# Kernel tuning notes

Measured on AMD Instinct MI355X. Metric: run time of the kernel, lower is better.

## Reference

```python
import jax, jax.numpy as jnp
import numpy as np

DIM = 1024
HEADS = 8
DIM_HEAD = 64
INNER = HEADS * DIM_HEAD  # 512
N_PATCHES = 256
SCALE = DIM_HEAD ** -0.5


def setup_inputs() -> dict:
    key = jax.random.key(0)
    ks = jax.random.split(key, 6)
    s = lambda fan_in: 1.0 / np.sqrt(fan_in)
    return {
        "x": jax.random.normal(ks[0], (64, N_PATCHES, DIM), dtype=jnp.float32),
        "Wq": jax.random.normal(ks[1], (DIM, INNER), dtype=jnp.float32) * s(DIM),
        "Wkv": jax.random.normal(ks[2], (DIM, 2 * INNER), dtype=jnp.float32) * s(DIM),
        "Wout": jax.random.normal(ks[3], (INNER, DIM), dtype=jnp.float32) * s(INNER),
        "bout": jax.random.normal(ks[4], (DIM,), dtype=jnp.float32) * 0.01,
        "Wspec": jax.random.normal(ks[5], (N_PATCHES, 3 * N_PATCHES), dtype=jnp.float32) * s(N_PATCHES),
    }


def reference(x, Wq, Wkv, Wout, bout, Wspec):
    b, n, d = x.shape
    # ---- spatial: single center-query attention ----
    x_center = x[:, n // 2, :]                      # [b, d]
    q = (x_center @ Wq).reshape(b, HEADS, DIM_HEAD)  # [b, h, dh]
    kv = x @ Wkv                                     # [b, n, 2*inner]
    k, v = jnp.split(kv, 2, axis=-1)
    k = k.reshape(b, n, HEADS, DIM_HEAD).transpose(0, 2, 1, 3)  # [b, h, n, dh]
    v = v.reshape(b, n, HEADS, DIM_HEAD).transpose(0, 2, 1, 3)
    logits = jnp.einsum('bhd,bhnd->bhn', q, k) * SCALE
    attn = jax.nn.softmax(logits, axis=-1)           # [b, h, n]
    out = jnp.einsum('bhn,bhnd->bhd', attn, v).reshape(b, INNER)
    # torch expands attn over n identical rows BEFORE to_out; the rows are
    # identical, so broadcasting the projected row is the same math.
    spatial = out @ Wout + bout                      # [b, d]
    spatial_out = jnp.broadcast_to(spatial[:, None, :], (b, n, d))
    # ---- spectral: attention over transposed (feature) axis ----
    x_t = x.transpose(0, 2, 1)                       # [b, d, n]
    qkv = x_t @ Wspec                                # [b, d, 3n]
    q_s, k_s, v_s = jnp.split(qkv, 3, axis=-1)       # v_s unused (as in source)
    spec_logits = jnp.einsum('bin,bjn->bij', q_s, k_s) * SCALE  # [b, d, d]
    spec_weights = jax.nn.softmax(spec_logits, axis=-1)
    return jnp.einsum('bnd,bde->bne', spatial_out, spec_weights)
```

## Files before the change

### kernel.cpp

```cpp
#include <hip/hip_runtime.h>
#include <hip/hip_bf16.h>
#include <cstdint>

typedef _Float16 f16;
typedef _Float16 half8 __attribute__((ext_vector_type(8)));
typedef float f32x4 __attribute__((ext_vector_type(4)));

#define SCALE 0.125f

#define GLL(src, dst) __builtin_amdgcn_global_load_lds( \
    (const __attribute__((address_space(1))) unsigned int*)(src), \
    (__attribute__((address_space(3))) unsigned int*)(dst), 16, 0, 0)

#define GLD(dst, addr) asm volatile("global_load_dwordx4 %0, %1, off" \
    : "=&v"(dst) : "v"(addr) : "memory")

__global__ __launch_bounds__(256) void prep_xT(const float* __restrict__ x, f16* __restrict__ xT) {
  __shared__ f16 tile[32][33];
  int b = blockIdx.z, nt = blockIdx.y, dt = blockIdx.x;
  int c = threadIdx.x & 31, rp = threadIdx.x >> 5;
  const float* xb = x + ((size_t)b*256 + nt*32)*1024 + dt*32;
#pragma unroll
  for (int p = 0; p < 4; ++p) { int r = p*8 + rp; tile[r][c] = (f16)xb[(size_t)r*1024 + c]; }
  __syncthreads();
  f16* o = xT + ((size_t)b*1024 + dt*32)*256 + nt*32;
#pragma unroll
  for (int p = 0; p < 4; ++p) { int r = p*8 + rp; o[(size_t)r*256 + c] = tile[c][r]; }
}

__global__ __launch_bounds__(256) void prep_Wspec16(const float* __restrict__ W, f16* __restrict__ Wt) {
  int row = blockIdx.x, t = threadIdx.x;
  Wt[(size_t)row*512 + t]       = (f16)W[(size_t)row*768 + t];
  Wt[(size_t)row*512 + 256 + t] = (f16)W[(size_t)row*768 + 256 + t];
}

template<int KSTEPS, int AST, int BST, int CST, bool SCALEQ>
__global__ __launch_bounds__(256) void gemm128(const f16* __restrict__ Ag, const f16* __restrict__ Bg,
                                               f16* __restrict__ Cg, size_t aB, size_t bB, size_t cB) {
  __shared__ f16 As[2][128*32];
  __shared__ f16 Bs[2][128*32];
  const f16* A = Ag + (size_t)blockIdx.z*aB;
  const f16* B = Bg + (size_t)blockIdx.z*bB;
  f16* C = Cg + (size_t)blockIdx.z*cB;
  int t = threadIdx.x, lane = t & 63, wave = t >> 6;
  int l15 = lane & 15, l4 = lane >> 4;
  int wm = wave & 1, wn = wave >> 1;
  size_t m0 = (size_t)blockIdx.x*128, n0 = (size_t)blockIdx.y*128;
  f32x4 acc[4][4];
#pragma unroll
  for (int i=0;i<4;++i)
#pragma unroll
    for (int j=0;j<4;++j) acc[i][j] = (f32x4){0.f,0.f,0.f,0.f};
  int rowS[2], chS[2];
#pragma unroll
  for (int c=0;c<2;++c) {
    int slot = c*256 + t;
    rowS[c] = slot >> 2;
    chS[c]  = (slot & 3) ^ ((slot >> 3) & 3);
  }
  int pc = (l4 ^ ((l15 >> 1) & 3)) * 8;

  auto STAGE = [&](int buf, int ks) {
    int k0 = ks*32;
#pragma unroll
    for (int c=0;c<2;++c) {
      GLL(A + (m0 + rowS[c])*(size_t)AST + k0 + chS[c]*8, &As[buf][(c*256 + wave*64)*8]);
      GLL(B + (n0 + rowS[c])*(size_t)BST + k0 + chS[c]*8, &Bs[buf][(c*256 + wave*64)*8]);
    }
  };

  STAGE(0, 0);
#pragma unroll 2
  for (int ks = 0; ks < KSTEPS; ++ks) {
    int cur = ks & 1;
    if (ks + 1 < KSTEPS) {
      STAGE(cur ^ 1, ks + 1);
      asm volatile("s_waitcnt vmcnt(4)" ::: "memory");
    } else {
      asm volatile("s_waitcnt vmcnt(0)" ::: "memory");
    }
    __builtin_amdgcn_s_barrier();
    __builtin_amdgcn_sched_barrier(0);
    half8 a[4], bb[4];
    const f16* Af = &As[cur][(wm*64 + l15)*32 + pc];
    const f16* Bf = &Bs[cur][(wn*64 + l15)*32 + pc];
#pragma unroll
    for (int mi=0;mi<4;++mi) a[mi]  = *(const half8*)(Af + mi*16*32);
#pragma unroll
    for (int ni=0;ni<4;++ni) bb[ni] = *(const half8*)(Bf + ni*16*32);
    __builtin_amdgcn_s_setprio(1);
#pragma unroll
    for (int mi=0;mi<4;++mi)
#pragma unroll
      for (int ni=0;ni<4;++ni)
        acc[mi][ni] = __builtin_amdgcn_mfma_f32_16x16x32_f16(a[mi], bb[ni], acc[mi][ni], 0,0,0);
    __builtin_amdgcn_s_setprio(0);
    __builtin_amdgcn_sched_barrier(0);
    __builtin_amdgcn_s_barrier();
  }
  float cscale = SCALEQ ? SCALE : 1.0f;
#pragma unroll
  for (int mi=0;mi<4;++mi)
#pragma unroll
    for (int ni=0;ni<4;++ni)
#pragma unroll
      for (int j=0;j<4;++j) {
        size_t row = m0 + wm*64 + mi*16 + 4*l4 + j;
        size_t col = n0 + wn*64 + ni*16 + l15;
        C[row*CST + col] = (f16)(acc[mi][ni][j] * cscale);
      }
}

__global__ __launch_bounds__(256) void qk(const float* __restrict__ x, const float* __restrict__ Wq,
                                          float* __restrict__ qbuf) {
  int b = blockIdx.x, h = blockIdx.y;
  int t = threadIdx.x;
  __shared__ float xc[1024];
  __shared__ float part[4][64];
  const float* xcg = x + ((size_t)b*256 + 128)*1024;
#pragma unroll
  for (int i = 0; i < 4; ++i) xc[t + 256*i] = xcg[t + 256*i];
  __syncthreads();
  int d = t & 63, chunk = t >> 6;
  float s = 0.f;
  const float* wq = Wq + (size_t)(chunk*256)*512 + h*64 + d;
#pragma unroll 8
  for (int c = 0; c < 256; ++c) s += xc[chunk*256 + c] * wq[(size_t)c*512];
  part[chunk][d] = s;
  __syncthreads();
  if (t < 64) qbuf[(size_t)b*512 + h*64 + t] = part[0][t]+part[1][t]+part[2][t]+part[3][t];
}

__global__ __launch_bounds__(256) void uk(const float* __restrict__ Wkv, const float* __restrict__ qbuf,
                                          f16* __restrict__ u16) {
  int h = blockIdx.x, dc = blockIdx.y;
  int t = threadIdx.x;
  __shared__ float Wk[32][64];
  __shared__ float qT[64][65];
  {
    int j = t & 63, g = t >> 6;
#pragma unroll
    for (int rr = 0; rr < 8; ++rr) {
      int dd = g*8 + rr;
      Wk[dd][j] = Wkv[(size_t)(dc*32 + dd)*1024 + h*64 + j];
    }
#pragma unroll
    for (int rr = 0; rr < 16; ++rr) {
      int bb = g*16 + rr;
      qT[j][bb] = qbuf[(size_t)bb*512 + h*64 + j];
    }
  }
  __syncthreads();
  int b = t & 63, dq = t >> 6;
#pragma unroll
  for (int i = 0; i < 8; ++i) {
    int dd = dq*8 + i;
    float s = 0.f;
#pragma unroll 8
    for (int j = 0; j < 64; ++j) s += qT[j][b] * Wk[dd][j];
    u16[((size_t)b*16 + h)*1024 + dc*32 + dd] = (f16)s;
  }
}

__global__ __launch_bounds__(64) void lgk(const float* __restrict__ x, const f16* __restrict__ u16,
                                          float* __restrict__ logitbuf) {
  int mt = blockIdx.x, b = blockIdx.y;
  int lane = threadIdx.x, l15 = lane & 15, l4 = lane >> 4;
  const float* Ap = x + ((size_t)b*256 + mt*16 + l15)*1024 + 8*l4;
  const f16* Bp = u16 + ((size_t)b*16 + l15)*1024 + 8*l4;
  f32x4 acc = (f32x4){0.f,0.f,0.f,0.f};
#pragma unroll 8
  for (int ks = 0; ks < 32; ++ks) {
    f32x4 lo = *(const f32x4*)(Ap + ks*32);
    f32x4 hi = *(const f32x4*)(Ap + ks*32 + 4);
    half8 h;
    h[0]=(f16)lo[0]; h[1]=(f16)lo[1]; h[2]=(f16)lo[2]; h[3]=(f16)lo[3];
    h[4]=(f16)hi[0]; h[5]=(f16)hi[1]; h[6]=(f16)hi[2]; h[7]=(f16)hi[3];
    acc = __builtin_amdgcn_mfma_f32_16x16x32_f16(h, *(const half8*)(Bp + ks*32), acc, 0,0,0);
  }
  if (l15 < 8) {
#pragma unroll
    for (int j = 0; j < 4; ++j)
      logitbuf[((size_t)b*256 + mt*16 + 4*l4 + j)*8 + l15] = acc[j];
  }
}

__global__ __launch_bounds__(256) void sm(const float* __restrict__ logitbuf, f16* __restrict__ attnW) {
  int b = blockIdx.x, t = threadIdx.x;
  __shared__ float eL[256][9];
  __shared__ float Zs[8];
  float e[8];
  const float* lp = logitbuf + (size_t)b*256*8 + (size_t)t*8;
#pragma unroll
  for (int h = 0; h < 8; ++h) { e[h] = __expf(lp[h] * SCALE); eL[t][h] = e[h]; }
  __syncthreads();
  {
    int h = t >> 5, i = t & 31;
    float s = 0.f;
#pragma unroll
    for (int k = 0; k < 8; ++k) s += eL[i + 32*k][h];
#pragma unroll
    for (int o = 1; o < 32; o <<= 1) s += __shfl_xor(s, o);
    if (i == 0) Zs[h] = s;
  }
  __syncthreads();
#pragma unroll
  for (int h = 0; h < 8; ++h) attnW[((size_t)b*16 + h)*256 + t] = (f16)(e[h] / Zs[h]);
#pragma unroll
  for (int h = 8; h < 16; ++h) attnW[((size_t)b*16 + h)*256 + t] = (f16)0.f;
}

__global__ __launch_bounds__(64) void xbk(const f16* __restrict__ attnW, const f16* __restrict__ xT,
                                          f16* __restrict__ xbar) {
  int dt = blockIdx.x, b = blockIdx.y;
  int lane = threadIdx.x, l15 = lane & 15, l4 = lane >> 4;
  const f16* Ap = attnW + ((size_t)b*16 + l15)*256 + 8*l4;
  const f16* Bp = xT + ((size_t)b*1024 + dt*16 + l15)*256 + 8*l4;
  f32x4 acc = (f32x4){0.f,0.f,0.f,0.f};
#pragma unroll
  for (int ks = 0; ks < 8; ++ks)
    acc = __builtin_amdgcn_mfma_f32_16x16x32_f16(*(const half8*)(Ap + ks*32),
                                                 *(const half8*)(Bp + ks*32), acc, 0,0,0);
  if (l4 < 2) {
#pragma unroll
    for (int j = 0; j < 4; ++j)
      xbar[((size_t)b*8 + 4*l4 + j)*1024 + dt*16 + l15] = (f16)acc[j];
  }
}

__global__ __launch_bounds__(256) void vk(const f16* __restrict__ xbar, const float* __restrict__ Wkv,
                                          float* __restrict__ attnout) {
  int h = blockIdx.x, dc = blockIdx.y, bc = blockIdx.z;
  int t = threadIdx.x;
  __shared__ float Wv[256][64];
  {
    int j = t & 63, g = t >> 6;
#pragma unroll
    for (int rr = 0; rr < 64; ++rr) {
      int dd = g*64 + rr;
      Wv[dd][j] = Wkv[(size_t)(dc*256 + dd)*1024 + 512 + h*64 + j];
    }
  }
  __syncthreads();
  int j = t & 63, bq = t >> 6;
  float s[4] = {0.f,0.f,0.f,0.f};
  const f16* xp[4];
#pragma unroll
  for (int bl = 0; bl < 4; ++bl)
    xp[bl] = xbar + ((size_t)(bc*16 + bq*4 + bl)*8 + h)*1024 + dc*256;
  for (int d8 = 0; d8 < 32; ++d8) {
    half8 xv[4];
#pragma unroll
    for (int bl = 0; bl < 4; ++bl) xv[bl] = *(const half8*)(xp[bl] + d8*8);
#pragma unroll
    for (int i = 0; i < 8; ++i) {
      float w = Wv[d8*8 + i][j];
#pragma unroll
      for (int bl = 0; bl < 4; ++bl) s[bl] += (float)xv[bl][i] * w;
    }
  }
#pragma unroll
  for (int bl = 0; bl < 4; ++bl)
    atomicAdd(&attnout[(size_t)(bc*16 + bq*4 + bl)*512 + h*64 + j], s[bl]);
}

__global__ __launch_bounds__(256) void spatialp(const float* __restrict__ attnout, const float* __restrict__ Wout,
                                                float* __restrict__ partial) {
  int ic = blockIdx.x, b = blockIdx.y;
  int t = threadIdx.x;
  __shared__ float ao[128];
  if (t < 128) ao[t] = attnout[(size_t)b*512 + ic*128 + t];
  __syncthreads();
  const float* W = Wout + (size_t)ic*128*1024 + t*4;
  f32x4 acc0 = (f32x4){0.f,0.f,0.f,0.f};
  f32x4 acc1 = (f32x4){0.f,0.f,0.f,0.f};
#pragma unroll 4
  for (int i = 0; i < 128; i += 2) {
    f32x4 w0 = *(const f32x4*)(W + (size_t)i*1024);
    f32x4 w1 = *(const f32x4*)(W + (size_t)(i+1)*1024);
    float a0 = ao[i], a1 = ao[i+1];
    acc0[0] += a0*w0[0]; acc0[1] += a0*w0[1]; acc0[2] += a0*w0[2]; acc0[3] += a0*w0[3];
    acc1[0] += a1*w1[0]; acc1[1] += a1*w1[1]; acc1[2] += a1*w1[2]; acc1[3] += a1*w1[3];
  }
  f32x4 acc;
#pragma unroll
  for (int j=0;j<4;++j) acc[j] = acc0[j] + acc1[j];
  *(f32x4*)(partial + ((size_t)(b*4 + ic))*1024 + t*4) = acc;
}

__global__ __launch_bounds__(256) void spatialr(const float* __restrict__ partial, const float* __restrict__ bout,
                                                float* __restrict__ spatial) {
  int b = blockIdx.x, t = threadIdx.x;
  f32x4 s = *(const f32x4*)(bout + t*4);
#pragma unroll
  for (int ic = 0; ic < 4; ++ic) {
    f32x4 p = *(const f32x4*)(partial + ((size_t)(b*4 + ic))*1024 + t*4);
#pragma unroll
    for (int j=0;j<4;++j) s[j] += p[j];
  }
  *(f32x4*)(spatial + (size_t)b*1024 + t*4) = s;
}

__global__ __launch_bounds__(512, 2) void speck(const f16* __restrict__ Y, const f16* __restrict__ xT,
                                                const float* __restrict__ spatial, float* __restrict__ r) {
  __shared__ f16 Bs[8][2][128*32];
  __shared__ __attribute__((aligned(16))) float sz[64*8];
  __shared__ float spat[64];
  int bid = blockIdx.x;
  int xcd = bid & 7, q = bid >> 3;
  int b = xcd*8 + (q >> 4);
  int iblk = q & 15;
  int t = threadIdx.x, lane = t & 63, wave = t >> 6;
  int l15 = lane & 15, l4 = lane >> 4;
  const f16* Yb  = Y  + (size_t)b*262144;
  const f16* xTb = xT + (size_t)b*262144;
  int i0 = iblk*64;
  if (t < 64) spat[t] = spatial[(size_t)b*1024 + i0 + t];

  f32x4 acc[4][8];
#pragma unroll
  for (int mi=0;mi<4;++mi)
#pragma unroll
    for (int ni=0;ni<8;++ni) acc[mi][ni] = (f32x4){0.f,0.f,0.f,0.f};
  int pc = (l4 ^ ((l15 >> 1) & 3)) * 8;
  int rowB = lane >> 2;
  int chB  = (lane & 3) ^ ((lane >> 3) & 3);

  half8 a[3][4];

  auto STAGE_B = [&](int ks) {
    int slot = ks & 1, k0 = ks*32;
#pragma unroll
    for (int c = 0; c < 8; ++c) {
      GLL(xTb + (size_t)(wave*128 + c*16 + rowB)*256 + k0 + chB*8,
          &Bs[wave][slot][c*512]);
    }
  };
  auto LOAD_A = [&](int ks, half8* dst) {
    int k0 = ks*32;
#pragma unroll
    for (int mi = 0; mi < 4; ++mi) {
      const f16* ap = Yb + (size_t)(i0 + mi*16 + l15)*256 + k0 + 8*l4;
      GLD(dst[mi], ap);
    }
  };

  LOAD_A(0, a[0]); STAGE_B(0); LOAD_A(1, a[1]); STAGE_B(1);
#pragma unroll
  for (int ks = 0; ks < 8; ++ks) {
    if (ks < 7) asm volatile("s_waitcnt vmcnt(12)" ::: "memory");
    else        asm volatile("s_waitcnt vmcnt(0)"  ::: "memory");
    __builtin_amdgcn_sched_barrier(0);
    half8 bb[8];
#pragma unroll
    for (int ni = 0; ni < 8; ++ni)
      bb[ni] = *(const half8*)(&Bs[wave][ks & 1][(ni*16 + l15)*32 + pc]);
    asm volatile("s_waitcnt lgkmcnt(0)" ::: "memory");
    __builtin_amdgcn_sched_barrier(0);
    if (ks < 6) { LOAD_A(ks + 2, a[(ks + 2) % 3]); STAGE_B(ks + 2); }
    __builtin_amdgcn_s_setprio(1);
#pragma unroll
    for (int ni = 0; ni < 8; ++ni)
#pragma unroll
      for (int mi = 0; mi < 4; ++mi)
        acc[mi][ni] = __builtin_amdgcn_mfma_f32_16x16x32_f16(a[ks % 3][mi], bb[ni], acc[mi][ni], 0,0,0);
    __builtin_amdgcn_s_setprio(0);
    __builtin_amdgcn_sched_barrier(0);
  }
#pragma unroll
  for (int mi=0;mi<4;++mi)
#pragma unroll
    for (int jj=0;jj<4;++jj) {
      float s = 0.f;
#pragma unroll
      for (int ni=0;ni<8;++ni) {
        float e = __expf(acc[mi][ni][jj]);
        acc[mi][ni][jj] = e;
        s += e;
      }
#pragma unroll
      for (int o=1;o<16;o<<=1) s += __shfl_xor(s, o);
      if (l15 == 0) sz[(mi*16 + 4*l4 + jj)*8 + wave] = s;
    }
  __syncthreads();
  float f[4][4];
#pragma unroll
  for (int mi=0;mi<4;++mi)
#pragma unroll
    for (int jj=0;jj<4;++jj) {
      int row = mi*16 + 4*l4 + jj;
      f32x4 lo = *(const f32x4*)(&sz[row*8]);
      f32x4 hi = *(const f32x4*)(&sz[row*8+4]);
      float zz = (lo[0]+lo[1]+lo[2]+lo[3]) + (hi[0]+hi[1]+hi[2]+hi[3]);
      f[mi][jj] = spat[row] / zz;
    }
  float* rb = r + (size_t)b*1024;
#pragma unroll
  for (int ni=0;ni<8;++ni) {
    float v = 0.f;
#pragma unroll
    for (int mi=0;mi<4;++mi)
#pragma unroll
      for (int jj=0;jj<4;++jj) v += f[mi][jj]*acc[mi][ni][jj];
    v += __shfl_xor(v, 16);
    v += __shfl_xor(v, 32);
    if (l4 == 0) atomicAdd(rb + wave*128 + ni*16 + l15, v);
  }
}

__global__ __launch_bounds__(256) void bcast(const float* __restrict__ r, float* __restrict__ out) {
  size_t row = blockIdx.x;
  int b = (int)(row >> 8);
  f32x4 v = *(const f32x4*)(r + (size_t)b*1024 + threadIdx.x*4);
  *(f32x4*)(out + row*1024 + (size_t)threadIdx.x*4) = v;
}

extern "C" void kernel_launch(void* const* d_in, const int* in_sizes, int n_in,
                              void* d_out, int out_size, void* d_ws, size_t ws_size,
                              hipStream_t stream) {
  const float* x     = (const float*)d_in[0];
  const float* Wq    = (const float*)d_in[1];
  const float* Wkv   = (const float*)d_in[2];
  const float* Wout  = (const float*)d_in[3];
  const float* bout  = (const float*)d_in[4];
  const float* Wspec = (const float*)d_in[5];
  float* out = (float*)d_out;
  char* ws = (char*)d_ws;
  f16*   Ybuf     = (f16*)(ws);
  f16*   u16pad   = (f16*)(ws);
  float* partial  = (float*)(ws);
  float* logitbuf = (float*)(ws + 2097152);
  f16*   attnW    = (f16*)(ws + 2621440);
  f16*   xbar     = (f16*)(ws + 3145728);
  float* qbuf     = (float*)(ws + 5242880);
  f16*   MT       = (f16*)(ws + 33554432);
  f16*   xT       = (f16*)(ws + 67108864);
  f16*   Wspec16  = (f16*)(ws + 102760448);
  float* attnout  = (float*)(ws + 103022592);
  float* spatial  = (float*)(ws + 103153664);
  float* rvec     = (float*)(ws + 103415808);
  (void)in_sizes; (void)n_in; (void)out_size; (void)ws_size;

  prep_xT     <<<dim3(32, 8, 64), dim3(256), 0, stream>>>(x, xT);
  prep_Wspec16<<<dim3(256),       dim3(256), 0, stream>>>(Wspec, Wspec16);
  gemm128<8,512,512,256,false><<<dim3(2, 2, 1), dim3(256), 0, stream>>>(Wspec16 + 256, Wspec16, MT, 0, 0, 0);
  hipMemsetAsync(u16pad, 0, 2097152, stream);
  hipMemsetAsync(attnout, 0, 64*512*sizeof(float), stream);
  qk          <<<dim3(64, 8),     dim3(256), 0, stream>>>(x, Wq, qbuf);
  uk          <<<dim3(8, 32),     dim3(256), 0, stream>>>(Wkv, qbuf, u16pad);
  lgk         <<<dim3(16, 64),    dim3(64),  0, stream>>>(x, u16pad, logitbuf);
  sm          <<<dim3(64),        dim3(256), 0, stream>>>(logitbuf, attnW);
  xbk         <<<dim3(64, 64),    dim3(64),  0, stream>>>(attnW, xT, xbar);
  vk          <<<dim3(8, 4, 4),   dim3(256), 0, stream>>>(xbar, Wkv, attnout);
  spatialp    <<<dim3(4, 64),     dim3(256), 0, stream>>>(attnout, Wout, partial);
  spatialr    <<<dim3(64),        dim3(256), 0, stream>>>(partial, bout, spatial);
  gemm128<8,256,256,256,true><<<dim3(8, 2, 64), dim3(256), 0, stream>>>(xT, MT, Ybuf,
                                                                        262144, 0, 262144);
  hipMemsetAsync(rvec, 0, 64*1024*sizeof(float), stream);
  speck       <<<dim3(1024),      dim3(512), 0, stream>>>(Ybuf, xT, spatial, rvec);
  bcast       <<<dim3(16384),     dim3(256), 0, stream>>>(rvec, out);
}
```

Before: 226.6 us.

## Widen speck to 16 waves with shared A tile staged in LDS

The speck kernel moves from 8 waves each covering 128 output columns to 16 waves each covering 64 columns, launched with 1024 threads. The 64x256 A tile (Y rows) is now loaded once into LDS with global_load_lds and shared by all waves, instead of each wave reading it from global memory into registers. The softmax denominator reduction becomes a two-level LDS reduction across 16 waves. The aim is more waves to hide latency and less redundant global traffic for A. In exchange it uses 160KB of LDS, adds extra barriers, and declares launch_bounds(1024,4), which that LDS size cannot actually deliver, so occupancy may be limited.

Measured after the change: 211.8 us. 1.07x faster.

```diff
diff --git a/kernel.cpp b/kernel.cpp
--- a/kernel.cpp
+++ b/kernel.cpp
@@ -11,9 +11,6 @@
 #define GLL(src, dst) __builtin_amdgcn_global_load_lds( \
     (const __attribute__((address_space(1))) unsigned int*)(src), \
     (__attribute__((address_space(3))) unsigned int*)(dst), 16, 0, 0)
-
-#define GLD(dst, addr) asm volatile("global_load_dwordx4 %0, %1, off" \
-    : "=&v"(dst) : "v"(addr) : "memory")
 
 __global__ __launch_bounds__(256) void prep_xT(const float* __restrict__ x, f16* __restrict__ xT) {
   __shared__ f16 tile[32][33];
@@ -301,11 +298,13 @@
   *(f32x4*)(spatial + (size_t)b*1024 + t*4) = s;
 }
 
-__global__ __launch_bounds__(512, 2) void speck(const f16* __restrict__ Y, const f16* __restrict__ xT,
-                                                const float* __restrict__ spatial, float* __restrict__ r) {
-  __shared__ f16 Bs[8][2][128*32];
-  __shared__ __attribute__((aligned(16))) float sz[64*8];
-  __shared__ float spat[64];
+__global__ __launch_bounds__(1024, 4) void speck(const f16* __restrict__ Y, const f16* __restrict__ xT,
+                                                 const float* __restrict__ spatial, float* __restrict__ r) {
+  __shared__ __attribute__((aligned(16))) char smem[163840];
+  f16* As = (f16*)smem;
+  f16* Bs = (f16*)(smem + 32768);
+  float* sz   = (float*)smem;
+  float* zfin = (float*)(smem + 4096);
   int bid = blockIdx.x;
   int xcd = bid & 7, q = bid >> 3;
   int b = xcd*8 + (q >> 4);
@@ -315,73 +314,91 @@
   const f16* Yb  = Y  + (size_t)b*262144;
   const f16* xTb = xT + (size_t)b*262144;
   int i0 = iblk*64;
-  if (t < 64) spat[t] = spatial[(size_t)b*1024 + i0 + t];
-
-  f32x4 acc[4][8];
+
+  f32x4 acc[4][4];
 #pragma unroll
   for (int mi=0;mi<4;++mi)
 #pragma unroll
-    for (int ni=0;ni<8;++ni) acc[mi][ni] = (f32x4){0.f,0.f,0.f,0.f};
+    for (int ni=0;ni<4;++ni) acc[mi][ni] = (f32x4){0.f,0.f,0.f,0.f};
   int pc = (l4 ^ ((l15 >> 1) & 3)) * 8;
-  int rowB = lane >> 2;
-  int chB  = (lane & 3) ^ ((lane >> 3) & 3);
-
-  half8 a[3][4];
-
-  auto STAGE_B = [&](int ks) {
-    int slot = ks & 1, k0 = ks*32;
-#pragma unroll
-    for (int c = 0; c < 8; ++c) {
-      GLL(xTb + (size_t)(wave*128 + c*16 + rowB)*256 + k0 + chB*8,
-          &Bs[wave][slot][c*512]);
+
+#pragma unroll
+  for (int g = 0; g < 2; ++g) {
+    int u = (wave*2 + g)*64 + lane;
+    int rA = u >> 5, v = u & 31, ksA = v >> 2, pchk = v & 3;
+    int ch = pchk ^ (((rA & 15) >> 1) & 3);
+    GLL(Yb + (size_t)(i0 + rA)*256 + ksA*32 + ch*8, As + ((wave*2 + g)*64)*8);
+  }
+  auto STAGE_B = [&](int slot, int ks) {
+    int k0 = ks*32;
+#pragma unroll
+    for (int c = 0; c < 4; ++c) {
+      int u2 = c*64 + lane;
+      int row = u2 >> 2, pchk = u2 & 3;
+      int ch = pchk ^ (((row & 15) >> 1) & 3);
+      GLL(xTb + (size_t)(wave*64 + row)*256 + k0 + ch*8,
+          Bs + ((wave*2 + slot)*256 + c*64)*8);
     }
   };
-  auto LOAD_A = [&](int ks, half8* dst) {
-    int k0 = ks*32;
-#pragma unroll
-    for (int mi = 0; mi < 4; ++mi) {
-      const f16* ap = Yb + (size_t)(i0 + mi*16 + l15)*256 + k0 + 8*l4;
-      GLD(dst[mi], ap);
-    }
-  };
-
-  LOAD_A(0, a[0]); STAGE_B(0); LOAD_A(1, a[1]); STAGE_B(1);
+  STAGE_B(0, 0);
+  STAGE_B(1, 1);
+  asm volatile("s_waitcnt vmcnt(8)" ::: "memory");
+  __builtin_amdgcn_s_barrier();
+
 #pragma unroll
   for (int ks = 0; ks < 8; ++ks) {
-    if (ks < 7) asm volatile("s_waitcnt vmcnt(12)" ::: "memory");
-    else        asm volatile("s_waitcnt vmcnt(0)"  ::: "memory");
+    int slot = ks & 1;
+    if (ks < 7) asm volatile("s_waitcnt vmcnt(4)" ::: "memory");
+    else        asm volatile("s_waitcnt vmcnt(0)" ::: "memory");
     __builtin_amdgcn_sched_barrier(0);
-    half8 bb[8];
-#pragma unroll
-    for (int ni = 0; ni < 8; ++ni)
-      bb[ni] = *(const half8*)(&Bs[wave][ks & 1][(ni*16 + l15)*32 + pc]);
+    half8 a[4], bb[4];
+    const f16* Bbase = Bs + (wave*2 + slot)*2048;
+#pragma unroll
+    for (int mi = 0; mi < 4; ++mi) a[mi]  = *(const half8*)(As + (mi*16 + l15)*256 + ks*32 + pc);
+#pragma unroll
+    for (int ni = 0; ni < 4; ++ni) bb[ni] = *(const half8*)(Bbase + (ni*16 + l15)*32 + pc);
     asm volatile("s_waitcnt lgkmcnt(0)" ::: "memory");
     __builtin_amdgcn_sched_barrier(0);
-    if (ks < 6) { LOAD_A(ks + 2, a[(ks + 2) % 3]); STAGE_B(ks + 2); }
+    if (ks < 6) STAGE_B(slot, ks + 2);
     __builtin_amdgcn_s_setprio(1);
 #pragma unroll
-    for (int ni = 0; ni < 8; ++ni)
+    for (int ni = 0; ni < 4; ++ni)
 #pragma unroll
       for (int mi = 0; mi < 4; ++mi)
-        acc[mi][ni] = __builtin_amdgcn_mfma_f32_16x16x32_f16(a[ks % 3][mi], bb[ni], acc[mi][ni], 0,0,0);
+        acc[mi][ni] = __builtin_amdgcn_mfma_f32_16x16x32_f16(a[mi], bb[ni], acc[mi][ni], 0,0,0);
     __builtin_amdgcn_s_setprio(0);
     __builtin_amdgcn_sched_barrier(0);
   }
+  float zr[4][4];
 #pragma unroll
   for (int mi=0;mi<4;++mi)
 #pragma unroll
     for (int jj=0;jj<4;++jj) {
       float s = 0.f;
 #pragma unroll
-      for (int ni=0;ni<8;++ni) {
+      for (int ni=0;ni<4;++ni) {
         float e = __expf(acc[mi][ni][jj]);
         acc[mi][ni][jj] = e;
         s += e;
       }
 #pragma unroll
       for (int o=1;o<16;o<<=1) s += __shfl_xor(s, o);
-      if (l15 == 0) sz[(mi*16 + 4*l4 + jj)*8 + wave] = s;
-    }
+      zr[mi][jj] = s;
+    }
+  __syncthreads();
+  if (l15 == 0) {
+#pragma unroll
+    for (int mi=0;mi<4;++mi)
+#pragma unroll
+      for (int jj=0;jj<4;++jj) sz[(mi*16 + 4*l4 + jj)*16 + wave] = zr[mi][jj];
+  }
+  __syncthreads();
+  {
+    float v = sz[t];
+#pragma unroll
+    for (int o=1;o<16;o<<=1) v += __shfl_xor(v, o);
+    if ((t & 15) == 0) zfin[t >> 4] = v;
+  }
   __syncthreads();
   float f[4][4];
 #pragma unroll
@@ -389,14 +406,11 @@
 #pragma unroll
     for (int jj=0;jj<4;++jj) {
       int row = mi*16 + 4*l4 + jj;
-      f32x4 lo = *(const f32x4*)(&sz[row*8]);
-      f32x4 hi = *(const f32x4*)(&sz[row*8+4]);
-      float zz = (lo[0]+lo[1]+lo[2]+lo[3]) + (hi[0]+hi[1]+hi[2]+hi[3]);
-      f[mi][jj] = spat[row] / zz;
+      f[mi][jj] = spatial[(size_t)b*1024 + i0 + row] / zfin[row];
     }
   float* rb = r + (size_t)b*1024;
 #pragma unroll
-  for (int ni=0;ni<8;++ni) {
+  for (int ni=0;ni<4;++ni) {
     float v = 0.f;
 #pragma unroll
     for (int mi=0;mi<4;++mi)
@@ -404,7 +418,7 @@
       for (int jj=0;jj<4;++jj) v += f[mi][jj]*acc[mi][ni][jj];
     v += __shfl_xor(v, 16);
     v += __shfl_xor(v, 32);
-    if (l4 == 0) atomicAdd(rb + wave*128 + ni*16 + l15, v);
+    if (l4 == 0) atomicAdd(rb + wave*64 + ni*16 + l15, v);
   }
 }
 
@@ -457,6 +471,6 @@
   gemm128<8,256,256,256,true><<<dim3(8, 2, 64), dim3(256), 0, stream>>>(xT, MT, Ybuf,
                                                                         262144, 0, 262144);
   hipMemsetAsync(rvec, 0, 64*1024*sizeof(float), stream);
-  speck       <<<dim3(1024),      dim3(512), 0, stream>>>(Ybuf, xT, spatial, rvec);
+  speck       <<<dim3(1024),      dim3(1024), 0, stream>>>(Ybuf, xT, spatial, rvec);
   bcast       <<<dim3(16384),     dim3(256), 0, stream>>>(rvec, out);
 }
```
